# Performance work log

Measured on AMD Instinct MI355X. Metric: run time of the kernel, lower is better.

## Reference

```python
import jax, jax.numpy as jnp
import numpy as np

HEADS = 8
DIM_HEAD = 64
ROPE_THETA = 10000.0


def _rope(t):
    # t: [b, h, n, d]; interleaved-pair rotation as in rotary-embedding-torch
    n, d = t.shape[-2], t.shape[-1]
    inv_freq = 1.0 / (ROPE_THETA ** (jnp.arange(0, d, 2, dtype=jnp.float32) / d))  # [d/2]
    freqs = jnp.arange(n, dtype=jnp.float32)[:, None] * inv_freq[None, :]  # [n, d/2]
    freqs = jnp.repeat(freqs, 2, axis=-1)  # [n, d], repeated per pair
    cos, sin = jnp.cos(freqs), jnp.sin(freqs)
    x1 = t[..., 0::2]
    x2 = t[..., 1::2]
    rot = jnp.stack((-x2, x1), axis=-1).reshape(t.shape)  # rotate_half
    return t * cos + rot * sin


def setup_inputs() -> dict:
    key = jax.random.key(0)
    k1, k2, k3, k4 = jax.random.split(key, 4)
    b, n, dim = 2, 2048, 512
    hidden = HEADS * DIM_HEAD
    x = jax.random.normal(k1, (b, n, dim), dtype=jnp.float32)
    pos_bias = jax.random.normal(k2, (HEADS, n, n), dtype=jnp.float32) * 0.02
    w_qkv = jax.random.normal(k3, (dim, 3 * hidden), dtype=jnp.float32) * (dim ** -0.5)
    w_out = jax.random.normal(k4, (hidden, dim), dtype=jnp.float32) * (hidden ** -0.5)
    return {"x": x, "pos_bias": pos_bias, "w_qkv": w_qkv, "w_out": w_out}


def reference(x, pos_bias, w_qkv, w_out):
    b, n, _ = x.shape
    qkv = x @ w_qkv  # [b, n, 3*hidden]
    q, k, v = jnp.split(qkv, 3, axis=-1)

    def to_heads(t):
        return t.reshape(b, n, HEADS, DIM_HEAD).transpose(0, 2, 1, 3)  # [b,h,n,d]

    q, k, v = map(to_heads, (q, k, v))
    k = _rope(k)
    q = _rope(q * (DIM_HEAD ** -0.5))
    sim = jnp.einsum('bhid,bhjd->bhij', q, k)  # [b,h,n,n]
    sim = sim + pos_bias  # broadcast over batch
    sim = sim - jax.lax.stop_gradient(jnp.max(sim, axis=-1, keepdims=True))
    attn = jax.nn.softmax(sim, axis=-1)
    out = jnp.einsum('bhij,bhjd->bhid', attn, v)
    out = out.transpose(0, 2, 1, 3).reshape(b, n, HEADS * DIM_HEAD)
    return out @ w_out
```

## Files before the change

### kernel.cpp

```cpp
#include <hip/hip_runtime.h>
#include <math.h>

#define SEQ 2048
#define NHEAD 8
#define HDIM 64
#define BATCH 2

typedef __attribute__((ext_vector_type(8))) short short8;
typedef __attribute__((ext_vector_type(4))) float f32x4;

__device__ __forceinline__ ushort f2bf(float f) {
    union { float f; unsigned u; } v; v.f = f;
    unsigned r = v.u + 0x7FFFu + ((v.u >> 16) & 1u);
    return (ushort)(r >> 16);
}

__device__ __forceinline__ f32x4 mfma16(short8 a, short8 b, f32x4 c) {
    return __builtin_amdgcn_mfma_f32_16x16x32_bf16(a, b, c, 0, 0, 0);
}

__device__ __forceinline__ void gld16(const void* g, void* l) {
    __builtin_amdgcn_global_load_lds(
        (const __attribute__((address_space(1))) unsigned int*)g,
        (__attribute__((address_space(3))) unsigned int*)l, 16, 0, 0);
}

__global__ __launch_bounds__(256)
void prep(const float* __restrict__ x, const float* __restrict__ w_qkv,
          const float* __restrict__ w_out, ushort* __restrict__ xb,
          ushort* __restrict__ wqkvT, ushort* __restrict__ woutT)
{
    __shared__ ushort tile[64][66];
    const int blk = blockIdx.x, t = threadIdx.x;
    if (blk < 1024) {
        const int i = (blk * 256 + t) * 8;
        float4 a = *(const float4*)&x[i];
        float4 b = *(const float4*)&x[i + 4];
        union { ushort us[8]; uint4 v; } pk;
        pk.us[0] = f2bf(a.x); pk.us[1] = f2bf(a.y); pk.us[2] = f2bf(a.z); pk.us[3] = f2bf(a.w);
        pk.us[4] = f2bf(b.x); pk.us[5] = f2bf(b.y); pk.us[6] = f2bf(b.z); pk.us[7] = f2bf(b.w);
        *(uint4*)&xb[i] = pk.v;
        return;
    }
    const float* w; ushort* wT; int K, N, n0, k0;
    if (blk < 1216) { const int s = blk - 1024; w = w_qkv; wT = wqkvT; K = 512; N = 1536; n0 = (s % 24) * 64; k0 = (s / 24) * 64; }
    else            { const int s = blk - 1216; w = w_out; wT = woutT; K = 512; N = 512;  n0 = (s % 8) * 64;  k0 = (s / 8) * 64; }
#pragma unroll
    for (int i = 0; i < 4; ++i) {
        const int slot = t + i * 256;
        const int r = slot >> 4, c4 = (slot & 15) * 4;
        float4 v = *(const float4*)&w[(size_t)(k0 + r) * N + n0 + c4];
        tile[c4 + 0][r] = f2bf(v.x);
        tile[c4 + 1][r] = f2bf(v.y);
        tile[c4 + 2][r] = f2bf(v.z);
        tile[c4 + 3][r] = f2bf(v.w);
    }
    __syncthreads();
    const int n = t >> 2, kc = (t & 3) * 16;
    union { ushort us[16]; uint4 v[2]; } o;
#pragma unroll
    for (int j = 0; j < 16; ++j) o.us[j] = tile[n][kc + j];
    *(uint4*)&wT[(size_t)(n0 + n) * K + k0 + kc]     = o.v[0];
    *(uint4*)&wT[(size_t)(n0 + n) * K + k0 + kc + 8] = o.v[1];
}

__global__ __launch_bounds__(256)
void gemm_qkv_rope(const ushort* __restrict__ xb, const ushort* __restrict__ wT,
                   ushort* __restrict__ qb, ushort* __restrict__ kb,
                   ushort* __restrict__ vtb)
{
    __shared__ __align__(16) ushort As[64][64];
    __shared__ __align__(16) ushort Bs[128][64];
    const int t = threadIdx.x, lane = t & 63, w = t >> 6;
    const int quad = lane >> 4, l16 = lane & 15;
    const int m0 = blockIdx.y * 64, n0 = blockIdx.x * 128;
    const int mw = (w >> 1) * 32, nw = (w & 1) * 64;
    const int krow = lane >> 3, kcol = (lane & 7) * 8;
    f32x4 acc[2][4] = {};

    for (int k0 = 0; k0 < 512; k0 += 64) {
        __syncthreads();
        gld16(&xb[(size_t)(m0 + w * 8 + krow) * 512 + k0 + kcol],        &As[w * 8][0]);
        gld16(&xb[(size_t)(m0 + (w + 4) * 8 + krow) * 512 + k0 + kcol],  &As[(w + 4) * 8][0]);
#pragma unroll
        for (int jj = 0; jj < 4; ++jj) {
            const int j = w * 4 + jj;
            gld16(&wT[(size_t)(n0 + j * 8 + krow) * 512 + k0 + kcol], &Bs[j * 8][0]);
        }
        __syncthreads();
#pragma unroll
        for (int ks = 0; ks < 2; ++ks) {
            short8 a[2], b[4];
#pragma unroll
            for (int i = 0; i < 2; ++i)
                a[i] = *(const short8*)&As[mw + i * 16 + l16][ks * 32 + quad * 8];
#pragma unroll
            for (int j = 0; j < 4; ++j)
                b[j] = *(const short8*)&Bs[nw + j * 16 + l16][ks * 32 + quad * 8];
#pragma unroll
            for (int i = 0; i < 2; ++i)
#pragma unroll
                for (int j = 0; j < 4; ++j)
                    acc[i][j] = mfma16(a[i], b[j], acc[i][j]);
        }
    }

    const int sec = (n0 + nw) >> 9;
    if (sec == 2) {
#pragma unroll
        for (int i = 0; i < 2; ++i) {
            const int m = m0 + mw + i * 16 + quad * 4;
            const int bidx = m >> 11, n = m & 2047;
#pragma unroll
            for (int j = 0; j < 4; ++j) {
                const int nc = n0 + nw + j * 16 + l16;
                const int d = nc & 63, h = (nc >> 6) & 7;
                ushort4 pk;
                pk.x = f2bf(acc[i][j][0]); pk.y = f2bf(acc[i][j][1]);
                pk.z = f2bf(acc[i][j][2]); pk.w = f2bf(acc[i][j][3]);
                *(ushort4*)&vtb[(((size_t)bidx * 8 + h) * 64 + d) * 2048 + n] = pk;
            }
        }
    } else {
        ushort* dst = (sec == 0) ? qb : kb;
        const float scale = (sec == 0) ? 0.125f : 1.0f;
#pragma unroll
        for (int j = 0; j < 4; ++j) {
            const int nc = n0 + nw + j * 16 + l16;
            const int d = nc & 63, h = (nc >> 6) & 7;
            const float inv = __expf(-(float)(d & ~1) * (9.2103403719761836f / 64.0f));
#pragma unroll
            for (int i = 0; i < 2; ++i)
#pragma unroll
            for (int r = 0; r < 4; ++r) {
                const int m = m0 + mw + i * 16 + quad * 4 + r;
                const int bidx = m >> 11, n = m & 2047;
                float sn, cs;
                __sincosf((float)n * inv, &sn, &cs);
                const float vacc = acc[i][j][r];
                const float partner = __shfl_xor(vacc, 1);
                const float rot = (d & 1) ? (vacc * cs + partner * sn)
                                          : (vacc * cs - partner * sn);
                dst[(((size_t)bidx * 8 + h) * 2048 + n) * 64 + d] = f2bf(rot * scale);
            }
        }
    }
}

__global__ __launch_bounds__(256)
void flash_attn_mfma(const ushort* __restrict__ qb, const ushort* __restrict__ kb,
                     const ushort* __restrict__ vtb, const float* __restrict__ bias,
                     ushort* __restrict__ ob)
{
    __shared__ __align__(16) ushort Ks[64][64];
    __shared__ __align__(16) ushort Vt[64][64];
    __shared__ __align__(16) float  Bl[64][64];
    __shared__ __align__(16) ushort Ps[4][16][72];
    const int t = threadIdx.x, lane = t & 63, w = t >> 6;
    const int quad = lane >> 4, l16 = lane & 15;
    const int q0 = blockIdx.x * 64, h = blockIdx.y, b = blockIdx.z;
    const size_t bh = (size_t)(b * NHEAD + h);
    const ushort* Q  = qb  + bh * SEQ * HDIM;
    const ushort* Kp = kb  + bh * SEQ * HDIM;
    const ushort* VT = vtb + bh * HDIM * SEQ;

    short8 qf[2];
    qf[0] = *(const short8*)&Q[(size_t)(q0 + w * 16 + l16) * HDIM + quad * 8];
    qf[1] = *(const short8*)&Q[(size_t)(q0 + w * 16 + l16) * HDIM + 32 + quad * 8];

    f32x4 oacc[4] = {};
    float lsum[4] = {};
    const int krow = lane >> 3, kcol = (lane & 7) * 8;
    const int brow = lane >> 4, bcol = (lane & 15) * 4;

    for (int it = 0; it < 32; ++it) {
        const int k0 = it * 64;
        __syncthreads();
        gld16(&Kp[(size_t)(k0 + w * 8 + krow) * HDIM + kcol],       &Ks[w * 8][0]);
        gld16(&Kp[(size_t)(k0 + (w + 4) * 8 + krow) * HDIM + kcol], &Ks[(w + 4) * 8][0]);
        gld16(&VT[(size_t)(w * 8 + krow) * SEQ + k0 + kcol],        &Vt[w * 8][0]);
        gld16(&VT[(size_t)((w + 4) * 8 + krow) * SEQ + k0 + kcol],  &Vt[(w + 4) * 8][0]);
#pragma unroll
        for (int jj = 0; jj < 4; ++jj) {
            const int j = w * 4 + jj;
            gld16(&bias[((size_t)h * SEQ + q0 + j * 4 + brow) * SEQ + k0 + bcol], &Bl[j * 4][0]);
        }
        __syncthreads();

        f32x4 sacc[4] = {};
#pragma unroll
        for (int ks = 0; ks < 2; ++ks)
#pragma unroll
            for (int s = 0; s < 4; ++s) {
                short8 kf = *(const short8*)&Ks[s * 16 + l16][ks * 32 + quad * 8];
                sacc[s] = mfma16(qf[ks], kf, sacc[s]);
            }

#pragma unroll
        for (int r = 0; r < 4; ++r)
#pragma unroll
            for (int s = 0; s < 4; ++s) {
                const float p = __expf(sacc[s][r] + Bl[w * 16 + quad * 4 + r][s * 16 + l16]);
                lsum[r] += p;
                Ps[w][quad * 4 + r][s * 16 + l16] = f2bf(p);
            }
        asm volatile("" ::: "memory");

#pragma unroll
        for (int ks = 0; ks < 2; ++ks) {
            short8 pf = *(const short8*)&Ps[w][l16][ks * 32 + quad * 8];
#pragma unroll
            for (int s = 0; s < 4; ++s) {
                short8 vf = *(const short8*)&Vt[s * 16 + l16][ks * 32 + quad * 8];
                oacc[s] = mfma16(pf, vf, oacc[s]);
            }
        }
    }

#pragma unroll
    for (int r = 0; r < 4; ++r) {
        float rs = lsum[r];
        rs += __shfl_xor(rs, 1, 16);
        rs += __shfl_xor(rs, 2, 16);
        rs += __shfl_xor(rs, 4, 16);
        rs += __shfl_xor(rs, 8, 16);
        const float invl = 1.0f / rs;
        const size_t m = (size_t)b * SEQ + q0 + w * 16 + quad * 4 + r;
#pragma unroll
        for (int s = 0; s < 4; ++s)
            ob[m * 512 + h * HDIM + s * 16 + l16] = f2bf(oacc[s][r] * invl);
    }
}

__global__ __launch_bounds__(256)
void gemm_out(const ushort* __restrict__ Ab, const ushort* __restrict__ wT,
              float* __restrict__ C)
{
    __shared__ __align__(16) ushort As[64][64];
    __shared__ __align__(16) ushort Bs[64][64];
    const int t = threadIdx.x, lane = t & 63, w = t >> 6;
    const int quad = lane >> 4, l16 = lane & 15;
    const int m0 = blockIdx.y * 64, n0 = blockIdx.x * 64;
    const int mw = (w >> 1) * 32, nw = (w & 1) * 32;
    const int krow = lane >> 3, kcol = (lane & 7) * 8;
    f32x4 acc[2][2] = {};

    for (int k0 = 0; k0 < 512; k0 += 64) {
        __syncthreads();
        gld16(&Ab[(size_t)(m0 + w * 8 + krow) * 512 + k0 + kcol],       &As[w * 8][0]);
        gld16(&Ab[(size_t)(m0 + (w + 4) * 8 + krow) * 512 + k0 + kcol], &As[(w + 4) * 8][0]);
        gld16(&wT[(size_t)(n0 + w * 8 + krow) * 512 + k0 + kcol],       &Bs[w * 8][0]);
        gld16(&wT[(size_t)(n0 + (w + 4) * 8 + krow) * 512 + k0 + kcol], &Bs[(w + 4) * 8][0]);
        __syncthreads();
#pragma unroll
        for (int ks = 0; ks < 2; ++ks) {
            short8 a[2], b[2];
#pragma unroll
            for (int i = 0; i < 2; ++i)
                a[i] = *(const short8*)&As[mw + i * 16 + l16][ks * 32 + quad * 8];
#pragma unroll
            for (int j = 0; j < 2; ++j)
                b[j] = *(const short8*)&Bs[nw + j * 16 + l16][ks * 32 + quad * 8];
#pragma unroll
            for (int i = 0; i < 2; ++i)
#pragma unroll
                for (int j = 0; j < 2; ++j)
                    acc[i][j] = mfma16(a[i], b[j], acc[i][j]);
        }
    }
#pragma unroll
    for (int i = 0; i < 2; ++i)
#pragma unroll
    for (int r = 0; r < 4; ++r) {
        const int m = m0 + mw + i * 16 + quad * 4 + r;
#pragma unroll
        for (int j = 0; j < 2; ++j)
            C[(size_t)m * 512 + n0 + nw + j * 16 + l16] = acc[i][j][r];
    }
}

extern "C" void kernel_launch(void* const* d_in, const int* in_sizes, int n_in,
                              void* d_out, int out_size, void* d_ws, size_t ws_size,
                              hipStream_t stream)
{
    const float* x        = (const float*)d_in[0];
    const float* pos_bias = (const float*)d_in[1];
    const float* w_qkv    = (const float*)d_in[2];
    const float* w_out    = (const float*)d_in[3];
    float* out = (float*)d_out;

    char* ws = (char*)d_ws;
    ushort* xb     = (ushort*)(ws);
    ushort* wqkvT  = (ushort*)(ws + 4194304);
    ushort* woutT  = (ushort*)(ws + 5767168);
    ushort* qb     = (ushort*)(ws + 6291456);
    ushort* kb     = (ushort*)(ws + 10485760);
    ushort* vtb    = (ushort*)(ws + 14680064);
    ushort* attnb  = (ushort*)(ws + 18874368);

    prep<<<1280, 256, 0, stream>>>(x, w_qkv, w_out, xb, wqkvT, woutT);
    gemm_qkv_rope<<<dim3(12, 64), 256, 0, stream>>>(xb, wqkvT, qb, kb, vtb);
    flash_attn_mfma<<<dim3(SEQ / 64, NHEAD, BATCH), 256, 0, stream>>>(qb, kb, vtb, pos_bias, attnb);
    gemm_out<<<dim3(8, 64), 256, 0, stream>>>(attnb, woutT, out);
}
```

Measured before the change: 257.2 us.

## Double-buffer LDS tiles and pre-swizzle global layouts to avoid bank conflicts

Adds ping-pong LDS buffers to the QKV GEMM, the attention loop and the output GEMM, so the next tile's global-to-LDS loads are issued before computing on the current tile, with one barrier per iteration. It also writes the intermediate bf16 tensors (x, transposed weights, K, V^T, attention output) in XOR-swizzled column order, so the direct global_load_lds copies land swizzled in LDS and the MFMA fragment reads avoid bank conflicts. The cost is doubled LDS use, which may lower occupancy in the attention kernel (about 48KB+), and more index arithmetic in the epilogue stores.

```diff
diff --git a/kernel.cpp b/kernel.cpp
--- a/kernel.cpp
+++ b/kernel.cpp
@@ -25,6 +25,13 @@
         (__attribute__((address_space(3))) unsigned int*)l, 16, 0, 0);
 }
 
+__device__ __forceinline__ int swz(int col, int row) {
+    return (col & ~63) | ((((col >> 3) ^ row) & 7) << 3) | (col & 7);
+}
+__device__ __forceinline__ int lswz(int cb, int row) {
+    return (((cb >> 3) ^ row) & 7) << 3;
+}
+
 __global__ __launch_bounds__(256)
 void prep(const float* __restrict__ x, const float* __restrict__ w_qkv,
           const float* __restrict__ w_out, ushort* __restrict__ xb,
@@ -34,12 +41,13 @@
     const int blk = blockIdx.x, t = threadIdx.x;
     if (blk < 1024) {
         const int i = (blk * 256 + t) * 8;
+        const int m = i >> 9, k = i & 511;
         float4 a = *(const float4*)&x[i];
         float4 b = *(const float4*)&x[i + 4];
         union { ushort us[8]; uint4 v; } pk;
         pk.us[0] = f2bf(a.x); pk.us[1] = f2bf(a.y); pk.us[2] = f2bf(a.z); pk.us[3] = f2bf(a.w);
         pk.us[4] = f2bf(b.x); pk.us[5] = f2bf(b.y); pk.us[6] = f2bf(b.z); pk.us[7] = f2bf(b.w);
-        *(uint4*)&xb[i] = pk.v;
+        *(uint4*)&xb[(size_t)m * 512 + swz(k, m)] = pk.v;
         return;
     }
     const float* w; ushort* wT; int K, N, n0, k0;
@@ -60,8 +68,9 @@
     union { ushort us[16]; uint4 v[2]; } o;
 #pragma unroll
     for (int j = 0; j < 16; ++j) o.us[j] = tile[n][kc + j];
-    *(uint4*)&wT[(size_t)(n0 + n) * K + k0 + kc]     = o.v[0];
-    *(uint4*)&wT[(size_t)(n0 + n) * K + k0 + kc + 8] = o.v[1];
+    const int ng = n0 + n;
+    *(uint4*)&wT[(size_t)ng * K + swz(k0 + kc, ng)]     = o.v[0];
+    *(uint4*)&wT[(size_t)ng * K + swz(k0 + kc + 8, ng)] = o.v[1];
 }
 
 __global__ __launch_bounds__(256)
@@ -69,8 +78,8 @@
                    ushort* __restrict__ qb, ushort* __restrict__ kb,
                    ushort* __restrict__ vtb)
 {
-    __shared__ __align__(16) ushort As[64][64];
-    __shared__ __align__(16) ushort Bs[128][64];
+    __shared__ __align__(16) ushort As[2][64][64];
+    __shared__ __align__(16) ushort Bs[2][128][64];
     const int t = threadIdx.x, lane = t & 63, w = t >> 6;
     const int quad = lane >> 4, l16 = lane & 15;
     const int m0 = blockIdx.y * 64, n0 = blockIdx.x * 128;
@@ -78,31 +87,42 @@
     const int krow = lane >> 3, kcol = (lane & 7) * 8;
     f32x4 acc[2][4] = {};
 
+    gld16(&xb[(size_t)(m0 + w * 8 + krow) * 512 + kcol],        &As[0][w * 8][0]);
+    gld16(&xb[(size_t)(m0 + (w + 4) * 8 + krow) * 512 + kcol],  &As[0][(w + 4) * 8][0]);
+#pragma unroll
+    for (int jj = 0; jj < 4; ++jj)
+        gld16(&wT[(size_t)(n0 + (w * 4 + jj) * 8 + krow) * 512 + kcol], &Bs[0][(w * 4 + jj) * 8][0]);
+    __syncthreads();
+
     for (int k0 = 0; k0 < 512; k0 += 64) {
-        __syncthreads();
-        gld16(&xb[(size_t)(m0 + w * 8 + krow) * 512 + k0 + kcol],        &As[w * 8][0]);
-        gld16(&xb[(size_t)(m0 + (w + 4) * 8 + krow) * 512 + k0 + kcol],  &As[(w + 4) * 8][0]);
-#pragma unroll
-        for (int jj = 0; jj < 4; ++jj) {
-            const int j = w * 4 + jj;
-            gld16(&wT[(size_t)(n0 + j * 8 + krow) * 512 + k0 + kcol], &Bs[j * 8][0]);
-        }
-        __syncthreads();
+        const int cur = (k0 >> 6) & 1;
+        if (k0 < 448) {
+            gld16(&xb[(size_t)(m0 + w * 8 + krow) * 512 + k0 + 64 + kcol],        &As[cur ^ 1][w * 8][0]);
+            gld16(&xb[(size_t)(m0 + (w + 4) * 8 + krow) * 512 + k0 + 64 + kcol],  &As[cur ^ 1][(w + 4) * 8][0]);
+#pragma unroll
+            for (int jj = 0; jj < 4; ++jj)
+                gld16(&wT[(size_t)(n0 + (w * 4 + jj) * 8 + krow) * 512 + k0 + 64 + kcol], &Bs[cur ^ 1][(w * 4 + jj) * 8][0]);
+        }
 #pragma unroll
         for (int ks = 0; ks < 2; ++ks) {
             short8 a[2], b[4];
 #pragma unroll
-            for (int i = 0; i < 2; ++i)
-                a[i] = *(const short8*)&As[mw + i * 16 + l16][ks * 32 + quad * 8];
-#pragma unroll
-            for (int j = 0; j < 4; ++j)
-                b[j] = *(const short8*)&Bs[nw + j * 16 + l16][ks * 32 + quad * 8];
+            for (int i = 0; i < 2; ++i) {
+                const int row = mw + i * 16 + l16;
+                a[i] = *(const short8*)&As[cur][row][lswz(ks * 32 + quad * 8, row)];
+            }
+#pragma unroll
+            for (int j = 0; j < 4; ++j) {
+                const int row = nw + j * 16 + l16;
+                b[j] = *(const short8*)&Bs[cur][row][lswz(ks * 32 + quad * 8, row)];
+            }
 #pragma unroll
             for (int i = 0; i < 2; ++i)
 #pragma unroll
                 for (int j = 0; j < 4; ++j)
                     acc[i][j] = mfma16(a[i], b[j], acc[i][j]);
         }
+        __syncthreads();
     }
 
     const int sec = (n0 + nw) >> 9;
@@ -118,7 +138,7 @@
                 ushort4 pk;
                 pk.x = f2bf(acc[i][j][0]); pk.y = f2bf(acc[i][j][1]);
                 pk.z = f2bf(acc[i][j][2]); pk.w = f2bf(acc[i][j][3]);
-                *(ushort4*)&vtb[(((size_t)bidx * 8 + h) * 64 + d) * 2048 + n] = pk;
+                *(ushort4*)&vtb[(((size_t)bidx * 8 + h) * 64 + d) * 2048 + swz(n, d)] = pk;
             }
         }
     } else {
@@ -141,7 +161,8 @@
                 const float partner = __shfl_xor(vacc, 1);
                 const float rot = (d & 1) ? (vacc * cs + partner * sn)
                                           : (vacc * cs - partner * sn);
-                dst[(((size_t)bidx * 8 + h) * 2048 + n) * 64 + d] = f2bf(rot * scale);
+                const int dcol = (sec == 0) ? d : swz(d, n);
+                dst[(((size_t)bidx * 8 + h) * 2048 + n) * 64 + dcol] = f2bf(rot * scale);
             }
         }
     }
@@ -152,9 +173,9 @@
                      const ushort* __restrict__ vtb, const float* __restrict__ bias,
                      ushort* __restrict__ ob)
 {
-    __shared__ __align__(16) ushort Ks[64][64];
-    __shared__ __align__(16) ushort Vt[64][64];
-    __shared__ __align__(16) float  Bl[64][64];
+    __shared__ __align__(16) ushort Ks[2][64][64];
+    __shared__ __align__(16) ushort Vt[2][64][64];
+    __shared__ __align__(16) float  Bl[2][64][64];
     __shared__ __align__(16) ushort Ps[4][16][72];
     const int t = threadIdx.x, lane = t & 63, w = t >> 6;
     const int quad = lane >> 4, l16 = lane & 15;
@@ -173,26 +194,36 @@
     const int krow = lane >> 3, kcol = (lane & 7) * 8;
     const int brow = lane >> 4, bcol = (lane & 15) * 4;
 
+    gld16(&Kp[(size_t)(w * 8 + krow) * HDIM + kcol],       &Ks[0][w * 8][0]);
+    gld16(&Kp[(size_t)((w + 4) * 8 + krow) * HDIM + kcol], &Ks[0][(w + 4) * 8][0]);
+    gld16(&VT[(size_t)(w * 8 + krow) * SEQ + kcol],        &Vt[0][w * 8][0]);
+    gld16(&VT[(size_t)((w + 4) * 8 + krow) * SEQ + kcol],  &Vt[0][(w + 4) * 8][0]);
+#pragma unroll
+    for (int jj = 0; jj < 4; ++jj)
+        gld16(&bias[((size_t)h * SEQ + q0 + (w * 4 + jj) * 4 + brow) * SEQ + bcol], &Bl[0][(w * 4 + jj) * 4][0]);
+    __syncthreads();
+
     for (int it = 0; it < 32; ++it) {
+        const int cur = it & 1;
         const int k0 = it * 64;
-        __syncthreads();
-        gld16(&Kp[(size_t)(k0 + w * 8 + krow) * HDIM + kcol],       &Ks[w * 8][0]);
-        gld16(&Kp[(size_t)(k0 + (w + 4) * 8 + krow) * HDIM + kcol], &Ks[(w + 4) * 8][0]);
-        gld16(&VT[(size_t)(w * 8 + krow) * SEQ + k0 + kcol],        &Vt[w * 8][0]);
-        gld16(&VT[(size_t)((w + 4) * 8 + krow) * SEQ + k0 + kcol],  &Vt[(w + 4) * 8][0]);
-#pragma unroll
-        for (int jj = 0; jj < 4; ++jj) {
-            const int j = w * 4 + jj;
-            gld16(&bias[((size_t)h * SEQ + q0 + j * 4 + brow) * SEQ + k0 + bcol], &Bl[j * 4][0]);
-        }
-        __syncthreads();
+        if (it < 31) {
+            const int kn = k0 + 64;
+            gld16(&Kp[(size_t)(kn + w * 8 + krow) * HDIM + kcol],       &Ks[cur ^ 1][w * 8][0]);
+            gld16(&Kp[(size_t)(kn + (w + 4) * 8 + krow) * HDIM + kcol], &Ks[cur ^ 1][(w + 4) * 8][0]);
+            gld16(&VT[(size_t)(w * 8 + krow) * SEQ + kn + kcol],        &Vt[cur ^ 1][w * 8][0]);
+            gld16(&VT[(size_t)((w + 4) * 8 + krow) * SEQ + kn + kcol],  &Vt[cur ^ 1][(w + 4) * 8][0]);
+#pragma unroll
+            for (int jj = 0; jj < 4; ++jj)
+                gld16(&bias[((size_t)h * SEQ + q0 + (w * 4 + jj) * 4 + brow) * SEQ + kn + bcol], &Bl[cur ^ 1][(w * 4 + jj) * 4][0]);
+        }
 
         f32x4 sacc[4] = {};
 #pragma unroll
         for (int ks = 0; ks < 2; ++ks)
 #pragma unroll
             for (int s = 0; s < 4; ++s) {
-                short8 kf = *(const short8*)&Ks[s * 16 + l16][ks * 32 + quad * 8];
+                const int row = s * 16 + l16;
+                short8 kf = *(const short8*)&Ks[cur][row][lswz(ks * 32 + quad * 8, row)];
                 sacc[s] = mfma16(qf[ks], kf, sacc[s]);
             }
 
@@ -200,7 +231,7 @@
         for (int r = 0; r < 4; ++r)
 #pragma unroll
             for (int s = 0; s < 4; ++s) {
-                const float p = __expf(sacc[s][r] + Bl[w * 16 + quad * 4 + r][s * 16 + l16]);
+                const float p = __expf(sacc[s][r] + Bl[cur][w * 16 + quad * 4 + r][s * 16 + l16]);
                 lsum[r] += p;
                 Ps[w][quad * 4 + r][s * 16 + l16] = f2bf(p);
             }
@@ -211,10 +242,12 @@
             short8 pf = *(const short8*)&Ps[w][l16][ks * 32 + quad * 8];
 #pragma unroll
             for (int s = 0; s < 4; ++s) {
-                short8 vf = *(const short8*)&Vt[s * 16 + l16][ks * 32 + quad * 8];
+                const int row = s * 16 + l16;
+                short8 vf = *(const short8*)&Vt[cur][row][lswz(ks * 32 + quad * 8, row)];
                 oacc[s] = mfma16(pf, vf, oacc[s]);
             }
         }
+        __syncthreads();
     }
 
 #pragma unroll
@@ -225,10 +258,12 @@
         rs += __shfl_xor(rs, 4, 16);
         rs += __shfl_xor(rs, 8, 16);
         const float invl = 1.0f / rs;
-        const size_t m = (size_t)b * SEQ + q0 + w * 16 + quad * 4 + r;
-#pragma unroll
-        for (int s = 0; s < 4; ++s)
-            ob[m * 512 + h * HDIM + s * 16 + l16] = f2bf(oacc[s][r] * invl);
+        const int m = b * SEQ + q0 + w * 16 + quad * 4 + r;
+#pragma unroll
+        for (int s = 0; s < 4; ++s) {
+            const int col = h * HDIM + s * 16 + l16;
+            ob[(size_t)m * 512 + swz(col, m)] = f2bf(oacc[s][r] * invl);
+        }
     }
 }
 
@@ -236,8 +271,8 @@
 void gemm_out(const ushort* __restrict__ Ab, const ushort* __restrict__ wT,
               float* __restrict__ C)
 {
-    __shared__ __align__(16) ushort As[64][64];
-    __shared__ __align__(16) ushort Bs[64][64];
+    __shared__ __align__(16) ushort As[2][64][64];
+    __shared__ __align__(16) ushort Bs[2][64][64];
     const int t = threadIdx.x, lane = t & 63, w = t >> 6;
     const int quad = lane >> 4, l16 = lane & 15;
     const int m0 = blockIdx.y * 64, n0 = blockIdx.x * 64;
@@ -245,28 +280,40 @@
     const int krow = lane >> 3, kcol = (lane & 7) * 8;
     f32x4 acc[2][2] = {};
 
+    gld16(&Ab[(size_t)(m0 + w * 8 + krow) * 512 + kcol],       &As[0][w * 8][0]);
+    gld16(&Ab[(size_t)(m0 + (w + 4) * 8 + krow) * 512 + kcol], &As[0][(w + 4) * 8][0]);
+    gld16(&wT[(size_t)(n0 + w * 8 + krow) * 512 + kcol],       &Bs[0][w * 8][0]);
+    gld16(&wT[(size_t)(n0 + (w + 4) * 8 + krow) * 512 + kcol], &Bs[0][(w + 4) * 8][0]);
+    __syncthreads();
+
     for (int k0 = 0; k0 < 512; k0 += 64) {
-        __syncthreads();
-        gld16(&Ab[(size_t)(m0 + w * 8 + krow) * 512 + k0 + kcol],       &As[w * 8][0]);
-        gld16(&Ab[(size_t)(m0 + (w + 4) * 8 + krow) * 512 + k0 + kcol], &As[(w + 4) * 8][0]);
-        gld16(&wT[(size_t)(n0 + w * 8 + krow) * 512 + k0 + kcol],       &Bs[w * 8][0]);
-        gld16(&wT[(size_t)(n0 + (w + 4) * 8 + krow) * 512 + k0 + kcol], &Bs[(w + 4) * 8][0]);
-        __syncthreads();
+        const int cur = (k0 >> 6) & 1;
+        if (k0 < 448) {
+            gld16(&Ab[(size_t)(m0 + w * 8 + krow) * 512 + k0 + 64 + kcol],       &As[cur ^ 1][w * 8][0]);
+            gld16(&Ab[(size_t)(m0 + (w + 4) * 8 + krow) * 512 + k0 + 64 + kcol], &As[cur ^ 1][(w + 4) * 8][0]);
+            gld16(&wT[(size_t)(n0 + w * 8 + krow) * 512 + k0 + 64 + kcol],       &Bs[cur ^ 1][w * 8][0]);
+            gld16(&wT[(size_t)(n0 + (w + 4) * 8 + krow) * 512 + k0 + 64 + kcol], &Bs[cur ^ 1][(w + 4) * 8][0]);
+        }
 #pragma unroll
         for (int ks = 0; ks < 2; ++ks) {
             short8 a[2], b[2];
 #pragma unroll
-            for (int i = 0; i < 2; ++i)
-                a[i] = *(const short8*)&As[mw + i * 16 + l16][ks * 32 + quad * 8];
-#pragma unroll
-            for (int j = 0; j < 2; ++j)
-                b[j] = *(const short8*)&Bs[nw + j * 16 + l16][ks * 32 + quad * 8];
+            for (int i = 0; i < 2; ++i) {
+                const int row = mw + i * 16 + l16;
+                a[i] = *(const short8*)&As[cur][row][lswz(ks * 32 + quad * 8, row)];
+            }
+#pragma unroll
+            for (int j = 0; j < 2; ++j) {
+                const int row = nw + j * 16 + l16;
+                b[j] = *(const short8*)&Bs[cur][row][lswz(ks * 32 + quad * 8, row)];
+            }
 #pragma unroll
             for (int i = 0; i < 2; ++i)
 #pragma unroll
                 for (int j = 0; j < 2; ++j)
                     acc[i][j] = mfma16(a[i], b[j], acc[i][j]);
         }
+        __syncthreads();
     }
 #pragma unroll
     for (int i = 0; i < 2; ++i)
```

After: 258.2 us. Within noise of the previous version (+0.4%).
